# Kernel tuning notes

Hardware: AMD Instinct MI355X
Metric: run time of the kernel (lower is better)

The kernel has to match this reference:

```python
import jax, jax.numpy as jnp
import numpy as np

N_SENT = 100000   # source ('sent') nodes
N_TYPE = 10000    # destination ('type') nodes
E = 640000        # edges of etype 'has'
D = 128           # out_dim
LEAKY_SLOPE = 0.01  # F.leaky_relu default


def setup_inputs() -> dict:
    key = jax.random.key(0)
    k0, k1, k2, k3, k4 = jax.random.split(key, 5)
    h_sent = jax.random.normal(k0, (N_SENT, D), jnp.float32)
    h_type = jax.random.normal(k1, (N_TYPE, D), jnp.float32)
    # attn_fc: Linear(2*D, 1, bias=False) -> weight [1, 2*D]
    attn_w = jax.random.normal(k2, (1, 2 * D), jnp.float32) * (1.0 / np.sqrt(2 * D))
    src_idx = jax.random.randint(k3, (E,), 0, N_SENT, dtype=jnp.int32)
    dst_idx = jax.random.randint(k4, (E,), 0, N_TYPE, dtype=jnp.int32)
    return {"h_sent": h_sent, "h_type": h_type, "attn_w": attn_w,
            "src_idx": src_idx, "dst_idx": dst_idx}


def reference(h_sent, h_type, attn_w, src_idx, dst_idx):
    w = attn_w[0]  # [2D]
    # attn_fc(cat(src_h, dst_h)) == src_h @ w[:D] + dst_h @ w[D:]  (no bias)
    s_src = h_sent @ w[:D]   # [N_SENT]
    s_dst = h_type @ w[D:]   # [N_TYPE]
    e = jax.nn.leaky_relu(s_src[src_idx] + s_dst[dst_idx], LEAKY_SLOPE)  # [E]
    # segment (per-destination) softmax over incoming edges
    m = jax.ops.segment_max(e, dst_idx, num_segments=N_TYPE)             # [N_TYPE]
    m = jnp.where(jnp.isfinite(m), m, 0.0)                               # empty segments -> 0
    ex = jnp.exp(e - m[dst_idx])                                         # [E]
    denom = jax.ops.segment_sum(ex, dst_idx, num_segments=N_TYPE)        # [N_TYPE]
    alpha = ex / denom[dst_idx]                                          # [E]
    # weighted scatter-sum of source features into destination nodes
    msg = alpha[:, None] * h_sent[src_idx]                               # [E, D]
    h_new = jax.ops.segment_sum(msg, dst_idx, num_segments=N_TYPE)       # [N_TYPE, D]
    # DGL only updates nodes that received messages; isolated nodes keep h
    deg = jax.ops.segment_sum(jnp.ones_like(e), dst_idx, num_segments=N_TYPE)
    return jnp.where(deg[:, None] > 0, h_new, h_type)
```

## Files before the change

kernel.cpp:

```cpp
#include <hip/hip_runtime.h>
#include <stdint.h>
#include <stddef.h>

#define N_SENT 100000
#define N_TYPE 10000
#define NEDGE  640000
#define NROWS  (N_SENT + N_TYPE)
#define MAXDEG 256
#define HB     64
#define HCHUNK (NEDGE / HB)

__device__ __forceinline__ float bf2f(uint32_t lo16) {
    return __builtin_bit_cast(float, lo16 << 16);
}
__device__ __forceinline__ uint32_t f2bf(float f) {
    uint32_t u = __builtin_bit_cast(uint32_t, f);
    return (u + 0x7fffu + ((u >> 16) & 1u)) >> 16;
}

__device__ __forceinline__ bool detect_bf16(const uint32_t* __restrict__ h) {
    uint32_t u = h[threadIdx.x & 63];
    uint32_t e_lo = (u >> 7) & 0xffu;
    int ok = (e_lo >= 100u && e_lo <= 140u) ? 1 : 0;
    unsigned long long m = __ballot(ok);
    return __popcll(m) >= 48;
}

#define SCORE_BLOCKS ((NROWS + 63) / 64)

__global__ __launch_bounds__(256) void scores_k(const void* __restrict__ h_sent,
                                                const void* __restrict__ h_type,
                                                const void* __restrict__ attn_w,
                                                float* __restrict__ s_src,
                                                float* __restrict__ s_dst) {
    int lane = threadIdx.x & 63;
    int r0   = (blockIdx.x * 4 + (int)(threadIdx.x >> 6)) * 16;
    bool isbf = detect_bf16((const uint32_t*)h_sent);
    float v[16];
    if (isbf) {
        uint32_t wv_s = ((const uint32_t*)attn_w)[lane];
        uint32_t wv_t = ((const uint32_t*)attn_w)[64 + lane];
        float ws0 = bf2f(wv_s & 0xffffu), ws1 = bf2f(wv_s >> 16);
        float wt0 = bf2f(wv_t & 0xffffu), wt1 = bf2f(wv_t >> 16);
        uint32_t hv[16];
#pragma unroll
        for (int i = 0; i < 16; i++) {
            int g  = r0 + i;
            int gc = g < NROWS ? g : NROWS - 1;
            bool isSrc = gc < N_SENT;
            const uint32_t* hp = isSrc
                ? (const uint32_t*)h_sent + (size_t)gc * 64
                : (const uint32_t*)h_type + (size_t)(gc - N_SENT) * 64;
            hv[i] = hp[lane];
        }
#pragma unroll
        for (int i = 0; i < 16; i++) {
            int g = r0 + i;
            bool isSrc = g < N_SENT;
            float wa = isSrc ? ws0 : wt0, wb = isSrc ? ws1 : wt1;
            v[i] = (g < NROWS)
                 ? (bf2f(hv[i] & 0xffffu) * wa + bf2f(hv[i] >> 16) * wb)
                 : 0.0f;
        }
    } else {
        float2 wv_s = ((const float2*)attn_w)[lane];
        float2 wv_t = ((const float2*)attn_w)[64 + lane];
        float2 hv[16];
#pragma unroll
        for (int i = 0; i < 16; i++) {
            int g  = r0 + i;
            int gc = g < NROWS ? g : NROWS - 1;
            bool isSrc = gc < N_SENT;
            const float2* hp = isSrc
                ? (const float2*)h_sent + (size_t)gc * 64
                : (const float2*)h_type + (size_t)(gc - N_SENT) * 64;
            hv[i] = hp[lane];
        }
#pragma unroll
        for (int i = 0; i < 16; i++) {
            int g = r0 + i;
            bool isSrc = g < N_SENT;
            float wa = isSrc ? wv_s.x : wv_t.x, wb = isSrc ? wv_s.y : wv_t.y;
            v[i] = (g < NROWS) ? (hv[i].x * wa + hv[i].y * wb) : 0.0f;
        }
    }
    int b0 = lane & 1, b1 = (lane >> 1) & 1, b2 = (lane >> 2) & 1, b3 = (lane >> 3) & 1;
    float w_[8];
#pragma unroll
    for (int i = 0; i < 8; i++) {
        float keep = b0 ? v[2 * i + 1] : v[2 * i];
        float send = b0 ? v[2 * i]     : v[2 * i + 1];
        w_[i] = keep + __shfl_xor(send, 1, 64);
    }
    float x_[4];
#pragma unroll
    for (int i = 0; i < 4; i++) {
        float keep = b1 ? w_[2 * i + 1] : w_[2 * i];
        float send = b1 ? w_[2 * i]     : w_[2 * i + 1];
        x_[i] = keep + __shfl_xor(send, 2, 64);
    }
    float y_[2];
#pragma unroll
    for (int i = 0; i < 2; i++) {
        float keep = b2 ? x_[2 * i + 1] : x_[2 * i];
        float send = b2 ? x_[2 * i]     : x_[2 * i + 1];
        y_[i] = keep + __shfl_xor(send, 4, 64);
    }
    float z;
    {
        float keep = b3 ? y_[1] : y_[0];
        float send = b3 ? y_[0] : y_[1];
        z = keep + __shfl_xor(send, 8, 64);
    }
    z += __shfl_xor(z, 16, 64);
    z += __shfl_xor(z, 32, 64);
    if (lane < 16) {
        int g = r0 + lane;
        if (g < NROWS) {
            if (g < N_SENT) s_src[g] = z;
            else            s_dst[g - N_SENT] = z;
        }
    }
}

__global__ __launch_bounds__(256) void count_k(const int* __restrict__ dst,
                                               uint32_t* __restrict__ count2) {
    __shared__ uint32_t hist[N_TYPE];
    int cb = blockIdx.x;
    int t  = threadIdx.x;
    for (int i = t; i < N_TYPE; i += 256) hist[i] = 0u;
    __syncthreads();
    int e0 = cb * HCHUNK;
    for (int i = t; i < HCHUNK; i += 256)
        atomicAdd(&hist[dst[e0 + i]], 1u);
    __syncthreads();
    uint32_t* row = count2 + (size_t)cb * N_TYPE;
    for (int i = t; i < N_TYPE; i += 256) row[i] = hist[i];
}

__global__ __launch_bounds__(256) void sumscan_k(uint32_t* __restrict__ count2,
                                                 uint32_t* __restrict__ total) {
    int b = blockIdx.x * 256 + (int)threadIdx.x;
    bool ok = b < N_TYPE;
    int bc = ok ? b : N_TYPE - 1;
    uint32_t vals[HB];
#pragma unroll
    for (int c = 0; c < HB; c++)
        vals[c] = count2[(size_t)c * N_TYPE + bc];
    uint32_t run = 0;
#pragma unroll
    for (int c = 0; c < HB; c++) { uint32_t v = vals[c]; vals[c] = run; run += v; }
    if (ok) {
        total[b] = run;
#pragma unroll
        for (int c = 0; c < HB; c++)
            count2[(size_t)c * N_TYPE + b] = vals[c];
    }
}

__global__ __launch_bounds__(1024) void scan_k(const uint32_t* __restrict__ total,
                                               uint32_t* __restrict__ offsets) {
    const int CH = 10;
    int t = threadIdx.x, lane = t & 63, wv = t >> 6;
    int base = t * CH;
    uint32_t local[CH];
    uint32_t tsum = 0;
#pragma unroll
    for (int i = 0; i < CH; i++) {
        int idx = base + i;
        uint32_t c = (idx < N_TYPE) ? total[idx] : 0u;
        local[i] = c;
        tsum += c;
    }
    uint32_t orig = tsum;
#pragma unroll
    for (int off = 1; off < 64; off <<= 1) {
        uint32_t v = __shfl_up(tsum, off, 64);
        if (lane >= off) tsum += v;
    }
    __shared__ uint32_t wsum[16];
    if (lane == 63) wsum[wv] = tsum;
    __syncthreads();
    if (wv == 0 && lane < 16) {
        uint32_t u = wsum[lane], o = u;
#pragma unroll
        for (int off = 1; off < 16; off <<= 1) {
            uint32_t v = __shfl_up(u, off, 64);
            if (lane >= off) u += v;
        }
        wsum[lane] = u - o;
    }
    __syncthreads();
    uint32_t run = wsum[wv] + tsum - orig;
#pragma unroll
    for (int i = 0; i < CH; i++) {
        int idx = base + i;
        if (idx < N_TYPE) {
            offsets[idx] = run;
            run += local[i];
        } else if (idx == N_TYPE) {
            offsets[idx] = run;
        }
    }
}

__global__ __launch_bounds__(256) void fill_k(const int* __restrict__ src,
                                              const int* __restrict__ dst,
                                              const uint32_t* __restrict__ offsets,
                                              const uint32_t* __restrict__ base2,
                                              uint32_t* __restrict__ edge_src) {
    __shared__ uint32_t cur[N_TYPE];
    int cb = blockIdx.x;
    int t  = threadIdx.x;
    const uint32_t* brow = base2 + (size_t)cb * N_TYPE;
    for (int i = t; i < N_TYPE; i += 256) cur[i] = offsets[i] + brow[i];
    __syncthreads();
    int e0 = cb * HCHUNK;
    for (int i = t; i < HCHUNK; i += 256) {
        int e = e0 + i;
        uint32_t pos = atomicAdd(&cur[dst[e]], 1u);
        edge_src[pos] = (uint32_t)src[e];
    }
}

__global__ __launch_bounds__(256) void agg_k(const void* __restrict__ h_sent,
                                             const void* __restrict__ h_type,
                                             const float* __restrict__ s_src,
                                             const float* __restrict__ s_dst,
                                             const uint32_t* __restrict__ offsets,
                                             const uint32_t* __restrict__ edge_src,
                                             void* __restrict__ out) {
    __shared__ float    sc[4][MAXDEG];
    __shared__ uint32_t ss[4][MAXDEG];
    int j     = (blockIdx.x * 256 + threadIdx.x) >> 6;
    int wslot = threadIdx.x >> 6;
    int lane  = threadIdx.x & 63;
    bool valid = j < N_TYPE;
    bool isbf  = detect_bf16((const uint32_t*)h_sent);
    uint32_t beg = 0, deg = 0;
    float sdj = 0.0f;
    if (valid) {
        beg = offsets[j];
        deg = offsets[j + 1] - beg;
        sdj = s_dst[j];
    }
    float*    mysc = sc[wslot];
    uint32_t* myss = ss[wslot];
    bool fits = (deg <= MAXDEG);
    float m = -INFINITY;
    for (uint32_t k = lane; k < deg; k += 64) {
        uint32_t s = edge_src[beg + k];
        float v = s_src[s] + sdj;
        v = v > 0.0f ? v : 0.01f * v;
        if (fits) { mysc[k] = v; myss[k] = s; }
        m = fmaxf(m, v);
    }
#pragma unroll
    for (int off = 32; off; off >>= 1) m = fmaxf(m, __shfl_xor(m, off, 64));
    __syncthreads();
    if (!valid) return;
    if (deg == 0) {
        if (isbf) ((uint32_t*)out)[(size_t)j * 64 + lane] =
                      ((const uint32_t*)h_type)[(size_t)j * 64 + lane];
        else      ((float2*)out)[(size_t)j * 64 + lane] =
                      ((const float2*)h_type)[(size_t)j * 64 + lane];
        return;
    }
    float denom = 0.0f, a0 = 0.0f, a1 = 0.0f;
    if (isbf) {
        const uint32_t* hp = (const uint32_t*)h_sent;
        uint32_t k = 0;
        if (fits) {
            for (; k + 8 <= deg; k += 8) {
                uint32_t sv[8]; float vv[8]; uint32_t gv[8];
#pragma unroll
                for (int i = 0; i < 8; i++) { sv[i] = myss[k + i]; vv[i] = mysc[k + i]; }
#pragma unroll
                for (int i = 0; i < 8; i++) gv[i] = hp[(size_t)sv[i] * 64 + lane];
#pragma unroll
                for (int i = 0; i < 8; i++) {
                    float w = __expf(vv[i] - m);
                    denom += w;
                    a0 += w * bf2f(gv[i] & 0xffffu);
                    a1 += w * bf2f(gv[i] >> 16);
                }
            }
            for (; k < deg; ++k) {
                float w = __expf(mysc[k] - m);
                uint32_t g = hp[(size_t)myss[k] * 64 + lane];
                denom += w;
                a0 += w * bf2f(g & 0xffffu);
                a1 += w * bf2f(g >> 16);
            }
        } else {
            for (k = 0; k < deg; ++k) {
                uint32_t s = edge_src[beg + k];
                float v = s_src[s] + sdj; v = v > 0.0f ? v : 0.01f * v;
                float w = __expf(v - m);
                uint32_t g = hp[(size_t)s * 64 + lane];
                denom += w;
                a0 += w * bf2f(g & 0xffffu);
                a1 += w * bf2f(g >> 16);
            }
        }
        float inv = 1.0f / denom;
        ((uint32_t*)out)[(size_t)j * 64 + lane] = f2bf(a0 * inv) | (f2bf(a1 * inv) << 16);
    } else {
        const float2* hp = (const float2*)h_sent;
        uint32_t k = 0;
        if (fits) {
            for (; k + 8 <= deg; k += 8) {
                uint32_t sv[8]; float vv[8]; float2 gv[8];
#pragma unroll
                for (int i = 0; i < 8; i++) { sv[i] = myss[k + i]; vv[i] = mysc[k + i]; }
#pragma unroll
                for (int i = 0; i < 8; i++) gv[i] = hp[(size_t)sv[i] * 64 + lane];
#pragma unroll
                for (int i = 0; i < 8; i++) {
                    float w = __expf(vv[i] - m);
                    denom += w;
                    a0 += w * gv[i].x;
                    a1 += w * gv[i].y;
                }
            }
            for (; k < deg; ++k) {
                float w = __expf(mysc[k] - m);
                float2 g = hp[(size_t)myss[k] * 64 + lane];
                denom += w;
                a0 += w * g.x;
                a1 += w * g.y;
            }
        } else {
            for (k = 0; k < deg; ++k) {
                uint32_t s = edge_src[beg + k];
                float v = s_src[s] + sdj; v = v > 0.0f ? v : 0.01f * v;
                float w = __expf(v - m);
                float2 g = hp[(size_t)s * 64 + lane];
                denom += w;
                a0 += w * g.x;
                a1 += w * g.y;
            }
        }
        float inv = 1.0f / denom;
        ((float2*)out)[(size_t)j * 64 + lane] = make_float2(a0 * inv, a1 * inv);
    }
}

static inline size_t align_up(size_t x) { return (x + 255) & ~(size_t)255; }

extern "C" void kernel_launch(void* const* d_in, const int* in_sizes, int n_in,
                              void* d_out, int out_size, void* d_ws, size_t ws_size,
                              hipStream_t stream) {
    const void* h_sent = d_in[0];
    const void* h_type = d_in[1];
    const void* attn_w = d_in[2];
    const int* src_idx = (const int*)d_in[3];
    const int* dst_idx = (const int*)d_in[4];

    char* w = (char*)d_ws;
    float*    s_src     = (float*)w;    w += align_up((size_t)N_SENT * 4);
    float*    s_dst     = (float*)w;    w += align_up((size_t)N_TYPE * 4);
    uint32_t* count2    = (uint32_t*)w; w += align_up((size_t)HB * N_TYPE * 4);
    uint32_t* total     = (uint32_t*)w; w += align_up((size_t)N_TYPE * 4);
    uint32_t* offsets   = (uint32_t*)w; w += align_up((size_t)(N_TYPE + 1) * 4);
    uint32_t* edge_src  = (uint32_t*)w; w += align_up((size_t)NEDGE * 4);

    scores_k<<<SCORE_BLOCKS, 256, 0, stream>>>(h_sent, h_type, attn_w, s_src, s_dst);
    count_k<<<HB, 256, 0, stream>>>(dst_idx, count2);
    sumscan_k<<<(N_TYPE + 255) / 256, 256, 0, stream>>>(count2, total);
    scan_k<<<1, 1024, 0, stream>>>(total, offsets);
    fill_k<<<HB, 256, 0, stream>>>(src_idx, dst_idx, offsets, count2, edge_src);
    agg_k<<<(N_TYPE + 3) / 4, 256, 0, stream>>>(h_sent, h_type, s_src, s_dst,
                                                offsets, edge_src, d_out);
}
```

Baseline: 188.2 us.

## Fuse histogram into scores kernel and fold offset scan into fill kernel

Merges the per-chunk destination histogram into the score kernel launch via extra leading blocks, and removes the single-block scan kernel by having each fill block recompute the exclusive scan of totals redundantly. Adds sched_barrier after the score loads to keep them batched. Aims to cut launch overhead and serialization between small kernels, at the cost of the scores blocks reserving a large shared histogram (lower occupancy) and redundant scan work with more registers in fill blocks.

```diff
diff --git a/kernel.cpp b/kernel.cpp
--- a/kernel.cpp
+++ b/kernel.cpp
@@ -28,13 +28,30 @@
 
 #define SCORE_BLOCKS ((NROWS + 63) / 64)
 
-__global__ __launch_bounds__(256) void scores_k(const void* __restrict__ h_sent,
-                                                const void* __restrict__ h_type,
-                                                const void* __restrict__ attn_w,
-                                                float* __restrict__ s_src,
-                                                float* __restrict__ s_dst) {
+__global__ __launch_bounds__(256) void scores_count_k(const void* __restrict__ h_sent,
+                                                      const void* __restrict__ h_type,
+                                                      const void* __restrict__ attn_w,
+                                                      const int* __restrict__ dst,
+                                                      float* __restrict__ s_src,
+                                                      float* __restrict__ s_dst,
+                                                      uint32_t* __restrict__ count2) {
+    __shared__ uint32_t hist[N_TYPE];
+    if (blockIdx.x < HB) {
+        int cb = blockIdx.x;
+        int t  = threadIdx.x;
+        for (int i = t; i < N_TYPE; i += 256) hist[i] = 0u;
+        __syncthreads();
+        int e0 = cb * HCHUNK;
+        for (int i = t; i < HCHUNK; i += 256)
+            atomicAdd(&hist[dst[e0 + i]], 1u);
+        __syncthreads();
+        uint32_t* row = count2 + (size_t)cb * N_TYPE;
+        for (int i = t; i < N_TYPE; i += 256) row[i] = hist[i];
+        return;
+    }
     int lane = threadIdx.x & 63;
-    int r0   = (blockIdx.x * 4 + (int)(threadIdx.x >> 6)) * 16;
+    int sb   = blockIdx.x - HB;
+    int r0   = (sb * 4 + (int)(threadIdx.x >> 6)) * 16;
     bool isbf = detect_bf16((const uint32_t*)h_sent);
     float v[16];
     if (isbf) {
@@ -53,6 +70,7 @@
                 : (const uint32_t*)h_type + (size_t)(gc - N_SENT) * 64;
             hv[i] = hp[lane];
         }
+        __builtin_amdgcn_sched_barrier(0);
 #pragma unroll
         for (int i = 0; i < 16; i++) {
             int g = r0 + i;
@@ -76,6 +94,7 @@
                 : (const float2*)h_type + (size_t)(gc - N_SENT) * 64;
             hv[i] = hp[lane];
         }
+        __builtin_amdgcn_sched_barrier(0);
 #pragma unroll
         for (int i = 0; i < 16; i++) {
             int g = r0 + i;
@@ -123,21 +142,6 @@
     }
 }
 
-__global__ __launch_bounds__(256) void count_k(const int* __restrict__ dst,
-                                               uint32_t* __restrict__ count2) {
-    __shared__ uint32_t hist[N_TYPE];
-    int cb = blockIdx.x;
-    int t  = threadIdx.x;
-    for (int i = t; i < N_TYPE; i += 256) hist[i] = 0u;
-    __syncthreads();
-    int e0 = cb * HCHUNK;
-    for (int i = t; i < HCHUNK; i += 256)
-        atomicAdd(&hist[dst[e0 + i]], 1u);
-    __syncthreads();
-    uint32_t* row = count2 + (size_t)cb * N_TYPE;
-    for (int i = t; i < N_TYPE; i += 256) row[i] = hist[i];
-}
-
 __global__ __launch_bounds__(256) void sumscan_k(uint32_t* __restrict__ count2,
                                                  uint32_t* __restrict__ total) {
     int b = blockIdx.x * 256 + (int)threadIdx.x;
@@ -158,10 +162,17 @@
     }
 }
 
-__global__ __launch_bounds__(1024) void scan_k(const uint32_t* __restrict__ total,
-                                               uint32_t* __restrict__ offsets) {
-    const int CH = 10;
-    int t = threadIdx.x, lane = t & 63, wv = t >> 6;
+__global__ __launch_bounds__(256) void fill_k(const int* __restrict__ src,
+                                              const int* __restrict__ dst,
+                                              const uint32_t* __restrict__ total,
+                                              const uint32_t* __restrict__ base2,
+                                              uint32_t* __restrict__ offsets,
+                                              uint32_t* __restrict__ edge_src) {
+    __shared__ uint32_t cur[N_TYPE];
+    __shared__ uint32_t wsum[4];
+    const int CH = 40;
+    int cb = blockIdx.x;
+    int t  = threadIdx.x, lane = t & 63, wv = t >> 6;
     int base = t * CH;
     uint32_t local[CH];
     uint32_t tsum = 0;
@@ -178,42 +189,23 @@
         uint32_t v = __shfl_up(tsum, off, 64);
         if (lane >= off) tsum += v;
     }
-    __shared__ uint32_t wsum[16];
     if (lane == 63) wsum[wv] = tsum;
     __syncthreads();
-    if (wv == 0 && lane < 16) {
-        uint32_t u = wsum[lane], o = u;
-#pragma unroll
-        for (int off = 1; off < 16; off <<= 1) {
-            uint32_t v = __shfl_up(u, off, 64);
-            if (lane >= off) u += v;
-        }
-        wsum[lane] = u - o;
-    }
-    __syncthreads();
-    uint32_t run = wsum[wv] + tsum - orig;
+    uint32_t wbase = 0;
+#pragma unroll
+    for (int w = 0; w < 4; w++) wbase += (w < wv) ? wsum[w] : 0u;
+    uint32_t run = wbase + tsum - orig;
+    const uint32_t* brow = base2 + (size_t)cb * N_TYPE;
 #pragma unroll
     for (int i = 0; i < CH; i++) {
         int idx = base + i;
         if (idx < N_TYPE) {
-            offsets[idx] = run;
-            run += local[i];
-        } else if (idx == N_TYPE) {
-            offsets[idx] = run;
-        }
-    }
-}
-
-__global__ __launch_bounds__(256) void fill_k(const int* __restrict__ src,
-                                              const int* __restrict__ dst,
-                                              const uint32_t* __restrict__ offsets,
-                                              const uint32_t* __restrict__ base2,
-                                              uint32_t* __restrict__ edge_src) {
-    __shared__ uint32_t cur[N_TYPE];
-    int cb = blockIdx.x;
-    int t  = threadIdx.x;
-    const uint32_t* brow = base2 + (size_t)cb * N_TYPE;
-    for (int i = t; i < N_TYPE; i += 256) cur[i] = offsets[i] + brow[i];
+            cur[idx] = run + brow[idx];
+            if (cb == 0) offsets[idx] = run;
+        }
+        run += local[i];
+    }
+    if (cb == 0 && t == 255) offsets[N_TYPE] = run;
     __syncthreads();
     int e0 = cb * HCHUNK;
     for (int i = t; i < HCHUNK; i += 256) {
@@ -365,11 +357,10 @@
     uint32_t* offsets   = (uint32_t*)w; w += align_up((size_t)(N_TYPE + 1) * 4);
     uint32_t* edge_src  = (uint32_t*)w; w += align_up((size_t)NEDGE * 4);
 
-    scores_k<<<SCORE_BLOCKS, 256, 0, stream>>>(h_sent, h_type, attn_w, s_src, s_dst);
-    count_k<<<HB, 256, 0, stream>>>(dst_idx, count2);
+    scores_count_k<<<HB + SCORE_BLOCKS, 256, 0, stream>>>(h_sent, h_type, attn_w,
+                                                          dst_idx, s_src, s_dst, count2);
     sumscan_k<<<(N_TYPE + 255) / 256, 256, 0, stream>>>(count2, total);
-    scan_k<<<1, 1024, 0, stream>>>(total, offsets);
-    fill_k<<<HB, 256, 0, stream>>>(src_idx, dst_idx, offsets, count2, edge_src);
+    fill_k<<<HB, 256, 0, stream>>>(src_idx, dst_idx, total, count2, offsets, edge_src);
     agg_k<<<(N_TYPE + 3) / 4, 256, 0, stream>>>(h_sent, h_type, s_src, s_dst,
                                                 offsets, edge_src, d_out);
 }
```

After: 197.0 us. +4.7%, slower.

## Quadruple histogram blocks and batch loads ahead of atomics in CSR build kernels

Applied to the files above, without the earlier changes.

Raises the number of histogram/fill blocks from 64 to 256, so each block handles 2500 edges and more CUs are occupied. The count and fill kernels now load all destination/source indices into registers before issuing the LDS atomics, with sched_barrier fences so the loads overlap. Per-block count rows and offset initialisation use uint4 vector accesses. sumscan processes the now-larger block dimension in groups of 64. The cost is four times more count2 storage and per-block row traffic: every block clears and writes a 10000-entry row, and the column scan reads and writes four times as much.

```diff
diff --git a/kernel.cpp b/kernel.cpp
--- a/kernel.cpp
+++ b/kernel.cpp
@@ -7,7 +7,7 @@
 #define NEDGE  640000
 #define NROWS  (N_SENT + N_TYPE)
 #define MAXDEG 256
-#define HB     64
+#define HB     256
 #define HCHUNK (NEDGE / HB)
 
 __device__ __forceinline__ float bf2f(uint32_t lo16) {
@@ -53,6 +53,7 @@
                 : (const uint32_t*)h_type + (size_t)(gc - N_SENT) * 64;
             hv[i] = hp[lane];
         }
+        __builtin_amdgcn_sched_barrier(0);
 #pragma unroll
         for (int i = 0; i < 16; i++) {
             int g = r0 + i;
@@ -76,6 +77,7 @@
                 : (const float2*)h_type + (size_t)(gc - N_SENT) * 64;
             hv[i] = hp[lane];
         }
+        __builtin_amdgcn_sched_barrier(0);
 #pragma unroll
         for (int i = 0; i < 16; i++) {
             int g = r0 + i;
@@ -128,14 +130,32 @@
     __shared__ uint32_t hist[N_TYPE];
     int cb = blockIdx.x;
     int t  = threadIdx.x;
-    for (int i = t; i < N_TYPE; i += 256) hist[i] = 0u;
+#pragma unroll
+    for (int i = 0; i < 40; i++) {
+        int idx = i * 256 + t;
+        if (idx < N_TYPE) hist[idx] = 0u;
+    }
     __syncthreads();
     int e0 = cb * HCHUNK;
-    for (int i = t; i < HCHUNK; i += 256)
-        atomicAdd(&hist[dst[e0 + i]], 1u);
-    __syncthreads();
-    uint32_t* row = count2 + (size_t)cb * N_TYPE;
-    for (int i = t; i < N_TYPE; i += 256) row[i] = hist[i];
+    int dv[10];
+#pragma unroll
+    for (int k = 0; k < 10; k++) {
+        int i = k * 256 + t;
+        dv[k] = dst[e0 + (i < HCHUNK ? i : HCHUNK - 1)];
+    }
+    __builtin_amdgcn_sched_barrier(0);
+#pragma unroll
+    for (int k = 0; k < 10; k++) {
+        int i = k * 256 + t;
+        if (i < HCHUNK) atomicAdd(&hist[dv[k]], 1u);
+    }
+    __syncthreads();
+    uint4* row = (uint4*)(count2 + (size_t)cb * N_TYPE);
+#pragma unroll
+    for (int i = 0; i < 10; i++) {
+        int idx = i * 256 + t;
+        if (idx < N_TYPE / 4) row[idx] = ((const uint4*)hist)[idx];
+    }
 }
 
 __global__ __launch_bounds__(256) void sumscan_k(uint32_t* __restrict__ count2,
@@ -143,19 +163,23 @@
     int b = blockIdx.x * 256 + (int)threadIdx.x;
     bool ok = b < N_TYPE;
     int bc = ok ? b : N_TYPE - 1;
-    uint32_t vals[HB];
-#pragma unroll
-    for (int c = 0; c < HB; c++)
-        vals[c] = count2[(size_t)c * N_TYPE + bc];
     uint32_t run = 0;
 #pragma unroll
-    for (int c = 0; c < HB; c++) { uint32_t v = vals[c]; vals[c] = run; run += v; }
-    if (ok) {
-        total[b] = run;
-#pragma unroll
-        for (int c = 0; c < HB; c++)
-            count2[(size_t)c * N_TYPE + b] = vals[c];
-    }
+    for (int g = 0; g < HB / 64; g++) {
+        uint32_t vals[64];
+#pragma unroll
+        for (int c = 0; c < 64; c++)
+            vals[c] = count2[(size_t)(g * 64 + c) * N_TYPE + bc];
+        __builtin_amdgcn_sched_barrier(0);
+#pragma unroll
+        for (int c = 0; c < 64; c++) { uint32_t v = vals[c]; vals[c] = run; run += v; }
+        if (ok) {
+#pragma unroll
+            for (int c = 0; c < 64; c++)
+                count2[(size_t)(g * 64 + c) * N_TYPE + b] = vals[c];
+        }
+    }
+    if (ok) total[b] = run;
 }
 
 __global__ __launch_bounds__(1024) void scan_k(const uint32_t* __restrict__ total,
@@ -213,13 +237,34 @@
     int cb = blockIdx.x;
     int t  = threadIdx.x;
     const uint32_t* brow = base2 + (size_t)cb * N_TYPE;
-    for (int i = t; i < N_TYPE; i += 256) cur[i] = offsets[i] + brow[i];
+#pragma unroll
+    for (int i = 0; i < 10; i++) {
+        int idx = i * 256 + t;
+        if (idx < N_TYPE / 4) {
+            uint4 o = ((const uint4*)offsets)[idx];
+            uint4 b = ((const uint4*)brow)[idx];
+            uint4 c; c.x = o.x + b.x; c.y = o.y + b.y; c.z = o.z + b.z; c.w = o.w + b.w;
+            ((uint4*)cur)[idx] = c;
+        }
+    }
     __syncthreads();
     int e0 = cb * HCHUNK;
-    for (int i = t; i < HCHUNK; i += 256) {
-        int e = e0 + i;
-        uint32_t pos = atomicAdd(&cur[dst[e]], 1u);
-        edge_src[pos] = (uint32_t)src[e];
+    int dv[10], sv[10];
+#pragma unroll
+    for (int k = 0; k < 10; k++) {
+        int i = k * 256 + t;
+        int e = e0 + (i < HCHUNK ? i : HCHUNK - 1);
+        dv[k] = dst[e];
+        sv[k] = src[e];
+    }
+    __builtin_amdgcn_sched_barrier(0);
+#pragma unroll
+    for (int k = 0; k < 10; k++) {
+        int i = k * 256 + t;
+        if (i < HCHUNK) {
+            uint32_t pos = atomicAdd(&cur[dv[k]], 1u);
+            edge_src[pos] = (uint32_t)sv[k];
+        }
     }
 }
 
```

New measurement: 175.0 us. 1.08x faster.
